# Optimization experiments

Measured on AMD Instinct MI355X. Metric: run time of the kernel, lower is better.

Reference implementation:

```python
import jax, jax.numpy as jnp
import numpy as np

N_NODES = 50000
N_EDGES = 800000
NODE_DIM = 27
HIDDEN = 64
CTX = 32
HEADS = 4
NEG_SLOPE = 0.2


def _gat_layer(x, src, dst, W, a_src, a_dst, bias, n_nodes):
    # x: [N, F_in], W: [F_in, H*C], a_src/a_dst: [H, C], bias: [C]
    h = (x @ W).reshape(n_nodes, HEADS, -1)            # [N, H, C]
    alpha_src = jnp.einsum('nhc,hc->nh', h, a_src)     # [N, H]
    alpha_dst = jnp.einsum('nhc,hc->nh', h, a_dst)     # [N, H]
    e = alpha_src[src] + alpha_dst[dst]                # [E, H]
    e = jax.nn.leaky_relu(e, NEG_SLOPE)
    # segment softmax over edges grouped by destination node
    e_max = jax.ops.segment_max(e, dst, num_segments=n_nodes)  # [N, H]
    e_exp = jnp.exp(e - e_max[dst])                    # [E, H]
    denom = jax.ops.segment_sum(e_exp, dst, num_segments=n_nodes)  # [N, H]
    alpha = e_exp / denom[dst]                         # [E, H]
    msg = alpha[:, :, None] * h[src]                   # [E, H, C]
    out = jax.ops.segment_sum(msg, dst, num_segments=n_nodes)      # [N, H, C]
    return out.mean(axis=1) + bias                     # concat=False -> head mean


def setup_inputs() -> dict:
    key = jax.random.key(0)
    ks = jax.random.split(key, 16)
    glorot = lambda k, shp: jax.random.normal(k, shp, jnp.float32) * jnp.sqrt(2.0 / (shp[0] + shp[-1]))
    inp = {
        'x': jax.random.normal(ks[0], (N_NODES, NODE_DIM), jnp.float32),
        'edge_index': jax.random.randint(ks[1], (2, N_EDGES), 0, N_NODES, jnp.int32),
        'donor_emb': jax.random.normal(ks[2], (1, CTX), jnp.float32),
        # GAT layer 1
        'W1': glorot(ks[3], (NODE_DIM, HEADS * HIDDEN)),
        'a_src1': glorot(ks[4], (HEADS, HIDDEN)),
        'a_dst1': glorot(ks[5], (HEADS, HIDDEN)),
        'b1': jnp.zeros((HIDDEN,), jnp.float32),
        # GAT layer 2
        'W2': glorot(ks[6], (HIDDEN, HEADS * HIDDEN)),
        'a_src2': glorot(ks[7], (HEADS, HIDDEN)),
        'a_dst2': glorot(ks[8], (HEADS, HIDDEN)),
        'b2': jnp.zeros((HIDDEN,), jnp.float32),
        # scorer MLP
        'Ws1': glorot(ks[9], (HIDDEN + CTX, HIDDEN)),
        'bs1': jnp.zeros((HIDDEN,), jnp.float32),
        'Ws2': glorot(ks[10], (HIDDEN, 1)),
        'bs2': jnp.zeros((1,), jnp.float32),
    }
    return inp


def reference(x, edge_index, donor_emb, W1, a_src1, a_dst1, b1,
              W2, a_src2, a_dst2, b2, Ws1, bs1, Ws2, bs2):
    n = x.shape[0]
    # PyG GATConv default add_self_loops=True
    loop = jnp.arange(n, dtype=edge_index.dtype)
    src = jnp.concatenate([edge_index[0], loop])
    dst = jnp.concatenate([edge_index[1], loop])

    h = jax.nn.elu(_gat_layer(x, src, dst, W1, a_src1, a_dst1, b1, n))
    h = jax.nn.elu(_gat_layer(h, src, dst, W2, a_src2, a_dst2, b2, n))

    ctx = jnp.concatenate([h, jnp.broadcast_to(donor_emb, (n, donor_emb.shape[-1]))], axis=-1)
    hidden = jax.nn.relu(ctx @ Ws1 + bs1)
    logits = (hidden @ Ws2 + bs2).squeeze(-1)          # [N]
    return logits
```

## Files before the change

### kernel.cpp

```cpp
#include <hip/hip_runtime.h>
#include <hip/hip_fp16.h>
#include <cmath>

#define HEADS 4
#define CH 64
#define HC 256
#define NEG 0.2f

typedef __attribute__((ext_vector_type(8))) short short8;
typedef __attribute__((ext_vector_type(4))) float f32x4;
typedef __fp16 half2_t __attribute__((ext_vector_type(2)));

__device__ __forceinline__ float leaky(float v){ return v > 0.f ? v : NEG * v; }

__device__ __forceinline__ short bf16_rne(float f){
    unsigned u = __float_as_uint(f);
    unsigned r = u + 0x7fffu + ((u >> 16) & 1u);
    return (short)(r >> 16);
}
__device__ __forceinline__ float bf16_to_f(short s){
    return __uint_as_float(((unsigned)(unsigned short)s) << 16);
}
__device__ __forceinline__ half2_t bc16(unsigned u){ return __builtin_bit_cast(half2_t, u); }
__device__ __forceinline__ unsigned packh2(float a, float b){
    __half ha = __float2half(a), hb = __float2half(b);
    return (unsigned)__builtin_bit_cast(unsigned short, ha)
         | ((unsigned)__builtin_bit_cast(unsigned short, hb) << 16);
}

__device__ __forceinline__ int block_excl_scan(int v, int* ws4){
    int tid = threadIdx.x, lane = tid & 63, wv = tid >> 6;
    int incl = v;
    #pragma unroll
    for (int off = 1; off < 64; off <<= 1){
        int t = __shfl_up(incl, off);
        if (lane >= off) incl += t;
    }
    if (lane == 63) ws4[wv] = incl;
    __syncthreads();
    int add = 0;
    for (int w = 0; w < wv; ++w) add += ws4[w];
    return incl - v + add;
}


__global__ __launch_bounds__(256) void prep_hist_kernel(
    const float* __restrict__ W1, const float* __restrict__ W2,
    const float* __restrict__ Ws1, const float* __restrict__ bs1,
    const float* __restrict__ donor,
    short* __restrict__ w1hi, short* __restrict__ w2hi,
    short* __restrict__ s1hi, short* __restrict__ s1lo,
    float* __restrict__ d1p,
    const int* __restrict__ ei, int E, int N, int NB, int* __restrict__ bucket_cnt)
{
    if ((int)blockIdx.x < 256){
        int t = blockIdx.x * 256 + threadIdx.x;
        int T = 256 * 256;
        for (int i = t; i < 256 * 40; i += T){
            int n = i / 40, k = i % 40;
            w1hi[i] = bf16_rne((k < 27) ? W1[(size_t)k * HC + n] : 0.f);
        }
        for (int i = t; i < 256 * 72; i += T){
            int n = i / 72, k = i % 72;
            w2hi[i] = bf16_rne((k < 64) ? W2[(size_t)k * HC + n] : 0.f);
        }
        for (int i = t; i < 64 * 72; i += T){
            int n = i / 72, k = i % 72;
            float v = (k < 64) ? Ws1[(size_t)k * 64 + n] : 0.f;
            short hi = bf16_rne(v);
            s1hi[i] = hi; s1lo[i] = bf16_rne(v - bf16_to_f(hi));
        }
        if (t < 64){
            float s = bs1[t];
            for (int k = 0; k < 32; ++k) s = fmaf(donor[k], Ws1[(size_t)(64 + k) * 64 + t], s);
            d1p[t] = s;
        }
    } else {
        __shared__ int lh[256];
        int tid = threadIdx.x;
        int ET = E + N;
        int ebase = ((int)blockIdx.x - 256) * 2048;
        lh[tid] = 0;
        __syncthreads();
        #pragma unroll
        for (int j = 0; j < 8; ++j){
            int e = ebase + j * 256 + tid;
            if (e < ET){
                int d = (e < E) ? ei[E + e] : (e - E);
                atomicAdd(&lh[d >> 8], 1);
            }
        }
        __syncthreads();
        if (tid < NB && lh[tid]) atomicAdd(&bucket_cnt[tid], lh[tid]);
    }
}


__global__ __launch_bounds__(256) void coarse_scatter_kernel(
    const int* __restrict__ ei, int E, int N, int NB,
    const int* __restrict__ bucket_cnt, int* __restrict__ bucket_cursor,
    unsigned* __restrict__ pairs)
{
    __shared__ int ws4[4];
    __shared__ int gbase[256];
    __shared__ int lh[256];
    __shared__ int gb[256];
    int tid = threadIdx.x;
    int ET = E + N;
    {
        int v = (tid < NB) ? bucket_cnt[tid] : 0;
        gbase[tid] = block_excl_scan(v, ws4);
    }
    lh[tid] = 0;
    __syncthreads();
    int ebase = blockIdx.x * 2048;
    int d[8], s[8], r[8];
    #pragma unroll
    for (int j = 0; j < 8; ++j){
        int e = ebase + j * 256 + tid;
        d[j] = -1;
        if (e < ET){
            if (e < E){ s[j] = ei[e]; d[j] = ei[E + e]; } else { s[j] = d[j] = e - E; }
            r[j] = atomicAdd(&lh[d[j] >> 8], 1);
        }
    }
    __syncthreads();
    if (tid < NB && lh[tid]) gb[tid] = gbase[tid] + atomicAdd(&bucket_cursor[tid], lh[tid]);
    __syncthreads();
    #pragma unroll
    for (int j = 0; j < 8; ++j){
        if (d[j] >= 0)
            pairs[gb[d[j] >> 8] + r[j]] = ((unsigned)d[j] << 16) | (unsigned)s[j];
    }
}


__device__ __forceinline__ void fine_sort_body(
    int b, const unsigned* __restrict__ pairs, const int* __restrict__ bucket_cnt, int NB,
    int* __restrict__ colsrc, int* __restrict__ rowptr, int N, int ET)
{
    __shared__ int ws4f[4];
    __shared__ int sb[257];
    __shared__ int hist[256];
    __shared__ int cur[256];
    int tid = threadIdx.x;
    {
        int v = (tid < NB) ? bucket_cnt[tid] : 0;
        int excl = block_excl_scan(v, ws4f);
        sb[tid] = excl;
        if (tid == 255) sb[256] = excl + v;
    }
    hist[tid] = 0;
    __syncthreads();
// ... 114 lines not shown
        }
    }

    #pragma unroll
    for (int r = 0; r < 4; ++r) {
        int n = n0 + wv * 16 + quad * 4 + r;
        if (n < N) {
            if (NT == 16) {
                #pragma unroll
                for (int q = 0; q < 4; ++q) {
                    uint2 u;
                    u.x = packh2(acc[q][r],     acc[q + 4][r]);
                    u.y = packh2(acc[q + 8][r], acc[q + 12][r]);
                    *(uint2*)((char*)h + (size_t)n * 512 + (q * 16 + ln) * 8) = u;
                }
            } else {
                #pragma unroll
                for (int q = 0; q < 4; ++q) {
                    unsigned u = packh2(acc[q][r], acc[q + 4][r]);
                    *(unsigned*)((char*)h + (size_t)n * 512 + (q * 16 + ln) * 8 + ((c0 >> 6) << 1)) = u;
                }
            }
        }
    }

    float aS[NT], aD[NT];
    #pragma unroll
    for (int nt = 0; nt < NT; ++nt) {
        aS[nt] = a_src[c0 + nt * 16 + ln];
        aD[nt] = a_dst[c0 + nt * 16 + ln];
    }
    #pragma unroll
    for (int hl = 0; hl < NT / 4; ++hl) {
        #pragma unroll
        for (int r = 0; r < 4; ++r) {
            float ps = 0.f, pd = 0.f;
            #pragma unroll
            for (int i = 0; i < 4; ++i) {
                ps = fmaf(acc[hl * 4 + i][r], aS[hl * 4 + i], ps);
                pd = fmaf(acc[hl * 4 + i][r], aD[hl * 4 + i], pd);
            }
            #pragma unroll
            for (int off = 1; off < 16; off <<= 1) {
                ps += __shfl_xor(ps, off);
                pd += __shfl_xor(pd, off);
            }
            if (ln == 0) {
                int n = n0 + wv * 16 + quad * 4 + r;
                if (n < N) {
                    int hg = c0 / 64 + hl;
                    asrc[n * 4 + hg] = ps;
                    adst[n * 4 + hg] = pd;
                }
            }
        }
    }
}

__global__ __launch_bounds__(256) void transform1_fine_kernel(
    const float* __restrict__ xin, const short* __restrict__ whi,
    const float* __restrict__ a_src, const float* __restrict__ a_dst,
    __half* __restrict__ h, float* __restrict__ asrc, float* __restrict__ adst, int N,
    int nblk, const unsigned* __restrict__ pairs, const int* __restrict__ bucket_cnt, int NB,
    int* __restrict__ colsrc, int* __restrict__ rowptr, int ET)
{
    if ((int)blockIdx.x < nblk) {
        transform_body<27, 1, 16, false, false>(blockIdx.x, 0, xin, whi, nullptr,
                                                a_src, a_dst, h, asrc, adst, N);
    } else {
        fine_sort_body(blockIdx.x - nblk, pairs, bucket_cnt, NB, colsrc, rowptr, N, ET);
    }
}

__global__ __launch_bounds__(256) void transform2_kernel(
    const float* __restrict__ xin, const short* __restrict__ whi,
    const float* __restrict__ a_src, const float* __restrict__ a_dst,
    __half* __restrict__ h, float* __restrict__ asrc, float* __restrict__ adst, int N)
{
    transform_body<64, 2, 16, false, true>(blockIdx.x, 0, xin, whi, nullptr,
                                           a_src, a_dst, h, asrc, adst, N);
}


__global__ __launch_bounds__(256) void aggregate_kernel(
    const int* __restrict__ rowptr, const int* __restrict__ colsrc,
    const __half* __restrict__ h, const float* __restrict__ asrc,
    const float* __restrict__ adst, const float* __restrict__ bias,
    float* __restrict__ hout, int N)
{
    int tid = threadIdx.x;
    int grp = tid >> 5;
    int lane32 = tid & 31;
    int n = blockIdx.x * 8 + grp;
    if (n >= N) return;
    int start = rowptr[n], end = rowptr[n + 1];
    int deg = end - start;
    const float4 ad = *(const float4*)(adst + (size_t)n * 4);

    int src0 = 0;
    float e0 = -1e30f, e1 = -1e30f, e2 = -1e30f, e3 = -1e30f;
    bool v0 = lane32 < deg;
    if (v0){
        src0 = colsrc[start + lane32];
        float4 as = *(const float4*)(asrc + (size_t)src0 * 4);
        e0 = leaky(as.x + ad.x); e1 = leaky(as.y + ad.y);
        e2 = leaky(as.z + ad.z); e3 = leaky(as.w + ad.w);
    }

    float m0, m1, m2, m3, i0, i1, i2, i3, p0, p1, p2, p3;
    if (deg <= 32){
        m0 = e0; m1 = e1; m2 = e2; m3 = e3;
        #pragma unroll
        for (int off = 1; off < 32; off <<= 1){
            m0 = fmaxf(m0, __shfl_xor(m0, off));
            m1 = fmaxf(m1, __shfl_xor(m1, off));
            m2 = fmaxf(m2, __shfl_xor(m2, off));
            m3 = fmaxf(m3, __shfl_xor(m3, off));
        }
        p0 = __expf(e0 - m0);
        p1 = __expf(e1 - m1);
        p2 = __expf(e2 - m2);
        p3 = __expf(e3 - m3);
        float t0 = p0, t1 = p1, t2 = p2, t3 = p3;
        #pragma unroll
        for (int off = 1; off < 32; off <<= 1){
            t0 += __shfl_xor(t0, off);
            t1 += __shfl_xor(t1, off);
            t2 += __shfl_xor(t2, off);
            t3 += __shfl_xor(t3, off);
        }
        i0 = 1.f / t0; i1 = 1.f / t1; i2 = 1.f / t2; i3 = 1.f / t3;
    } else {
        m0 = e0; m1 = e1; m2 = e2; m3 = e3;
        float t0 = v0 ? 1.f : 0.f, t1 = t0, t2 = t0, t3 = t0;
        for (int i = start + 32 + lane32; i < end; i += 32){
            int s = colsrc[i];
            float4 as = *(const float4*)(asrc + (size_t)s * 4);
            float e, nm;
            e = leaky(as.x + ad.x); nm = fmaxf(m0, e); t0 = t0 * __expf(m0 - nm) + __expf(e - nm); m0 = nm;
            e = leaky(as.y + ad.y); nm = fmaxf(m1, e); t1 = t1 * __expf(m1 - nm) + __expf(e - nm); m1 = nm;
            e = leaky(as.z + ad.z); nm = fmaxf(m2, e); t2 = t2 * __expf(m2 - nm) + __expf(e - nm); m2 = nm;
            e = leaky(as.w + ad.w); nm = fmaxf(m3, e); t3 = t3 * __expf(m3 - nm) + __expf(e - nm); m3 = nm;
        }
        #pragma unroll
        for (int off = 1; off < 32; off <<= 1){
            float om, os, nm;
            om = __shfl_xor(m0, off); os = __shfl_xor(t0, off);
            nm = fmaxf(m0, om); t0 = t0 * __expf(m0 - nm) + os * __expf(om - nm); m0 = nm;
            om = __shfl_xor(m1, off); os = __shfl_xor(t1, off);
            nm = fmaxf(m1, om); t1 = t1 * __expf(m1 - nm) + os * __expf(om - nm); m1 = nm;
            om = __shfl_xor(m2, off); os = __shfl_xor(t2, off);
            nm = fmaxf(m2, om); t2 = t2 * __expf(m2 - nm) + os * __expf(om - nm); m2 = nm;
            om = __shfl_xor(m3, off); os = __shfl_xor(t3, off);
            nm = fmaxf(m3, om); t3 = t3 * __expf(m3 - nm) + os * __expf(om - nm); m3 = nm;
        }
        i0 = 1.f / t0; i1 = 1.f / t1; i2 = 1.f / t2; i3 = 1.f / t3;
        p0 = __expf(e0 - m0); p1 = __expf(e1 - m1);
        p2 = __expf(e2 - m2); p3 = __expf(e3 - m3);
    }

    float accA = 0.f, accB = 0.f;
    const int boff = lane32 * 16;
    bool first = true;
    for (int base = start; base < end; base += 32){
        int cnt = end - base; if (cnt > 32) cnt = 32;
        float w0, w1, w2, w3; int off = 0;
        if (first){
            w0 = p0 * i0; w1 = p1 * i1; w2 = p2 * i2; w3 = p3 * i3;
            off = v0 ? src0 * (HC * 2) : 0;
        } else {
            w0 = w1 = w2 = w3 = 0.f;
            if (lane32 < cnt){
                int s = colsrc[base + lane32];
                float4 as = *(const float4*)(asrc + (size_t)s * 4);
                w0 = __expf(leaky(as.x + ad.x) - m0) * i0;
                w1 = __expf(leaky(as.y + ad.y) - m1) * i1;
                w2 = __expf(leaky(as.z + ad.z) - m2) * i2;
                w3 = __expf(leaky(as.w + ad.w) - m3) * i3;
                off = s * (HC * 2);
            }
        }
        first = false;
        half2_t q01 = __builtin_amdgcn_cvt_pkrtz(w0, w1);
        half2_t q23 = __builtin_amdgcn_cvt_pkrtz(w2, w3);
        unsigned wx = __builtin_bit_cast(unsigned, q01);
        unsigned wy = __builtin_bit_cast(unsigned, q23);

        int j = 0;
        for (; j + 2 <= cnt; j += 2){
            int o0 = __shfl(off, j, 32);
            unsigned a0 = __shfl((int)wx, j, 32), b0 = __shfl((int)wy, j, 32);
            int o1 = __shfl(off, j + 1, 32);
            unsigned a1 = __shfl((int)wx, j + 1, 32), b1 = __shfl((int)wy, j + 1, 32);
            uint4 h0 = *(const uint4*)((const char*)h + o0 + boff);
            uint4 h1 = *(const uint4*)((const char*)h + o1 + boff);
            accA = __builtin_amdgcn_fdot2(bc16(h0.x), bc16(a0), accA, false);
            accA = __builtin_amdgcn_fdot2(bc16(h0.y), bc16(b0), accA, false);
            accB = __builtin_amdgcn_fdot2(bc16(h0.z), bc16(a0), accB, false);
            accB = __builtin_amdgcn_fdot2(bc16(h0.w), bc16(b0), accB, false);
            accA = __builtin_amdgcn_fdot2(bc16(h1.x), bc16(a1), accA, false);
            accA = __builtin_amdgcn_fdot2(bc16(h1.y), bc16(b1), accA, false);
            accB = __builtin_amdgcn_fdot2(bc16(h1.z), bc16(a1), accB, false);
            accB = __builtin_amdgcn_fdot2(bc16(h1.w), bc16(b1), accB, false);
        }
        for (; j < cnt; ++j){
            int o0 = __shfl(off, j, 32);
            unsigned a0 = __shfl((int)wx, j, 32), b0 = __shfl((int)wy, j, 32);
            uint4 h0 = *(const uint4*)((const char*)h + o0 + boff);
            accA = __builtin_amdgcn_fdot2(bc16(h0.x), bc16(a0), accA, false);
            accA = __builtin_amdgcn_fdot2(bc16(h0.y), bc16(b0), accA, false);
            accB = __builtin_amdgcn_fdot2(bc16(h0.z), bc16(a0), accB, false);
            accB = __builtin_amdgcn_fdot2(bc16(h0.w), bc16(b0), accB, false);
        }
    }

    float2 bv = *(const float2*)(bias + lane32 * 2);
    float oA = accA * 0.25f + bv.x;
    float oB = accB * 0.25f + bv.y;
    oA = (oA > 0.f) ? oA : expm1f(oA);
    oB = (oB > 0.f) ? oB : expm1f(oB);
    *(float2*)(hout + (size_t)n * CH + lane32 * 2) = make_float2(oA, oB);
}


__global__ __launch_bounds__(256) void scorer_mfma_kernel(
    const float* __restrict__ h2, const short* __restrict__ s1hi, const short* __restrict__ s1lo,
    const float* __restrict__ d1p, const float* __restrict__ Ws2, const float* __restrict__ bs2,
    float* __restrict__ out, int N)
{
    constexpr int WP = 72;
    __shared__ short whi[64 * WP];
    __shared__ short wlo[64 * WP];
    const int tid = threadIdx.x;
    const int n0 = blockIdx.x * 64;

    const int wv = tid >> 6, lane = tid & 63;
    const int quad = lane >> 4, ln = lane & 15;
    const int myrow = wv * 16 + ln;
    const int nme = n0 + myrow;

    float fdir[16];
    #pragma unroll
    for (int ks = 0; ks < 2; ++ks){
        float4 f0 = make_float4(0.f, 0.f, 0.f, 0.f), f1 = f0;
        if (nme < N){
            const float* ap = h2 + (size_t)nme * 64 + ks * 32 + quad * 8;
            f0 = *(const float4*)ap;
            f1 = *(const float4*)(ap + 4);
        }
        fdir[ks*8+0]=f0.x; fdir[ks*8+1]=f0.y; fdir[ks*8+2]=f0.z; fdir[ks*8+3]=f0.w;
        fdir[ks*8+4]=f1.x; fdir[ks*8+5]=f1.y; fdir[ks*8+6]=f1.z; fdir[ks*8+7]=f1.w;
    }
    {
        const short8* ghi = (const short8*)s1hi;
        const short8* glo = (const short8*)s1lo;
        short8* lhi = (short8*)whi;
        short8* llo = (short8*)wlo;
        for (int t = tid; t < 64 * WP / 8; t += 256){ lhi[t] = ghi[t]; llo[t] = glo[t]; }
    }
    __syncthreads();

    f32x4 acc[4];
    #pragma unroll
    for (int i = 0; i < 4; ++i) acc[i] = (f32x4){0.f, 0.f, 0.f, 0.f};

    #pragma unroll
    for (int ks = 0; ks < 2; ++ks) {
        const int k0 = ks * 32 + quad * 8;
        short8 ahi, alo;
        #pragma unroll
        for (int e = 0; e < 8; ++e) {
            float v = fdir[ks * 8 + e];
            short hi = bf16_rne(v);
            ahi[e] = hi;
            alo[e] = bf16_rne(v - bf16_to_f(hi));
        }
        #pragma unroll
        for (int nt = 0; nt < 4; ++nt) {
            short8 bhi = *(const short8*)(whi + (nt * 16 + ln) * WP + k0);
            short8 blo = *(const short8*)(wlo + (nt * 16 + ln) * WP + k0);
            acc[nt] = __builtin_amdgcn_mfma_f32_16x16x32_bf16(ahi, bhi, acc[nt], 0, 0, 0);
            acc[nt] = __builtin_amdgcn_mfma_f32_16x16x32_bf16(alo, bhi, acc[nt], 0, 0, 0);
            acc[nt] = __builtin_amdgcn_mfma_f32_16x16x32_bf16(ahi, blo, acc[nt], 0, 0, 0);
        }
    }

    float d1v[4], w2v[4];
    #pragma unroll
    for (int nt = 0; nt < 4; ++nt){
        d1v[nt] = d1p[nt * 16 + ln];
        w2v[nt] = Ws2[nt * 16 + ln];
    }
    float b2 = bs2[0];
    #pragma unroll
    for (int r = 0; r < 4; ++r){
        float t = 0.f;
        #pragma unroll
        for (int nt = 0; nt < 4; ++nt)
            t = fmaf(fmaxf(acc[nt][r] + d1v[nt], 0.f), w2v[nt], t);
        #pragma unroll
        for (int off = 1; off < 16; off <<= 1) t += __shfl_xor(t, off);
        if (ln == 0){
            int n = n0 + wv * 16 + quad * 4 + r;
            if (n < N) out[n] = t + b2;
        }
    }
}


extern "C" void kernel_launch(void* const* d_in, const int* in_sizes, int n_in,
                              void* d_out, int out_size, void* d_ws, size_t ws_size,
                              hipStream_t stream)
{
    const float* x    = (const float*)d_in[0];
    const int*   ei   = (const int*)  d_in[1];
    const float* donor= (const float*)d_in[2];
    const float* W1   = (const float*)d_in[3];
    const float* as1  = (const float*)d_in[4];
    const float* ad1  = (const float*)d_in[5];
    const float* b1   = (const float*)d_in[6];
    const float* W2   = (const float*)d_in[7];
    const float* as2  = (const float*)d_in[8];
    const float* ad2  = (const float*)d_in[9];
    const float* b2   = (const float*)d_in[10];
    const float* Ws1  = (const float*)d_in[11];
    const float* bs1  = (const float*)d_in[12];
    const float* Ws2  = (const float*)d_in[13];
    const float* bs2  = (const float*)d_in[14];

    const int N  = in_sizes[0] / 27;
    const int E  = in_sizes[1] / 2;
    const int ET = E + N;
    const int NB = (N + 255) / 256;

    char* ws = (char*)d_ws;
    auto alloc = [&](size_t bytes) -> void* {
        void* p = (void*)ws;
        ws += (bytes + 255) / 256 * 256;
        return p;
    };
    int*      rowptr  = (int*)     alloc((size_t)(N + 1) * 4);
    int*      colsrc  = (int*)     alloc((size_t)ET * 4);
    unsigned* pairs   = (unsigned*)alloc((size_t)ET * 4);
    __half*   hbig    = (__half*)  alloc((size_t)N * HC * 2);
    float*    asrc    = (float*)   alloc((size_t)N * 4 * 4);
    float*    adst    = (float*)   alloc((size_t)N * 4 * 4);
    float*    hmid    = (float*)   alloc((size_t)N * CH * 4);
    int*      bucket_cnt    = (int*) alloc(256 * 4);
    int*      bucket_cursor = (int*) alloc(256 * 4);
    short*    w1hi    = (short*)   alloc(256 * 40 * 2);
    short*    w2hi    = (short*)   alloc(256 * 72 * 2);
    short*    s1hi    = (short*)   alloc(64 * 72 * 2);
    short*    s1lo    = (short*)   alloc(64 * 72 * 2);
    float*    d1p     = (float*)   alloc(64 * 4);

    const int nblk = (N + 63) / 64;
    const int hblk = (ET + 2047) / 2048;

    (void)hipMemsetAsync(bucket_cnt, 0, 512 * 4, stream);
    prep_hist_kernel<<<256 + hblk, 256, 0, stream>>>(W1, W2, Ws1, bs1, donor,
        w1hi, w2hi, s1hi, s1lo, d1p, ei, E, N, NB, bucket_cnt);
    coarse_scatter_kernel<<<hblk, 256, 0, stream>>>(ei, E, N, NB, bucket_cnt, bucket_cursor, pairs);
    transform1_fine_kernel<<<nblk + NB, 256, 0, stream>>>(
        x, w1hi, as1, ad1, hbig, asrc, adst, N,
        nblk, pairs, bucket_cnt, NB, colsrc, rowptr, ET);
    aggregate_kernel<<<(N + 7) / 8, 256, 0, stream>>>(
        rowptr, colsrc, hbig, asrc, adst, b1, hmid, N);
    transform2_kernel<<<nblk, 256, 0, stream>>>(
        hmid, w2hi, as2, ad2, hbig, asrc, adst, N);
    aggregate_kernel<<<(N + 7) / 8, 256, 0, stream>>>(
        rowptr, colsrc, hbig, asrc, adst, b2, hmid, N);
    scorer_mfma_kernel<<<nblk, 256, 0, stream>>>(
        hmid, s1hi, s1lo, d1p, Ws2, bs2, (float*)d_out, N);
}
```

Baseline: 285.6 us.

## Prefetch neighbor rows into LDS with async ring buffer in aggregate

For nodes with degree at most 32, the aggregate kernel now uses global_load_lds to stream gathered neighbor feature rows into a per-wave 8-slot LDS ring. Manual vmcnt and lgkmcnt waits keep up to eight gathers in flight while earlier rows are read back and accumulated with fdot2. It also splits accumulation into two independent chains and computes normalized weights directly. The intent is to hide the latency of the irregular gathers, at the cost of hand-written wait counts, extra LDS use per block and wasted prefetches past the end of short neighbor lists.

```diff
diff --git a/kernel.cpp b/kernel.cpp
--- a/kernel.cpp
+++ b/kernel.cpp
@@ -10,6 +10,9 @@
 typedef __attribute__((ext_vector_type(8))) short short8;
 typedef __attribute__((ext_vector_type(4))) float f32x4;
 typedef __fp16 half2_t __attribute__((ext_vector_type(2)));
+typedef __attribute__((address_space(3))) char lds_char_t;
+typedef __attribute__((address_space(3))) void lds_void_t;
+typedef const __attribute__((address_space(1))) void g_void_t;
 
 __device__ __forceinline__ float leaky(float v){ return v > 0.f ? v : NEG * v; }
 
@@ -26,6 +29,18 @@
     __half ha = __float2half(a), hb = __float2half(b);
     return (unsigned)__builtin_bit_cast(unsigned short, ha)
          | ((unsigned)__builtin_bit_cast(unsigned short, hb) << 16);
+}
+__device__ __forceinline__ float fd2(unsigned hv, unsigned w, float acc){
+    return __builtin_amdgcn_fdot2(bc16(hv), bc16(w), acc, false);
+}
+
+__device__ __forceinline__ void gload_lds16(const void* g, void* l){
+    __builtin_amdgcn_global_load_lds((g_void_t*)g, (lds_void_t*)l, 16, 0, 0);
+}
+__device__ __forceinline__ uint4 lds_read_b128(unsigned addr){
+    uint4 r;
+    asm volatile("ds_read_b128 %0, %1" : "=v"(r) : "v"(addr));
+    return r;
 }
 
 __device__ __forceinline__ int block_excl_scan(int v, int* ws4){
@@ -355,7 +370,10 @@
     const float* __restrict__ adst, const float* __restrict__ bias,
     float* __restrict__ hout, int N)
 {
+    __shared__ char stage[4][8 * 1024];
     int tid = threadIdx.x;
+    int wv = tid >> 6;
+    int lane = tid & 63;
     int grp = tid >> 5;
     int lane32 = tid & 31;
     int n = blockIdx.x * 8 + grp;
@@ -374,9 +392,11 @@
         e2 = leaky(as.z + ad.z); e3 = leaky(as.w + ad.w);
     }
 
-    float m0, m1, m2, m3, i0, i1, i2, i3, p0, p1, p2, p3;
+    float accA = 0.f, accB = 0.f;
+    const int boff = lane32 * 16;
+
     if (deg <= 32){
-        m0 = e0; m1 = e1; m2 = e2; m3 = e3;
+        float m0 = e0, m1 = e1, m2 = e2, m3 = e3;
         #pragma unroll
         for (int off = 1; off < 32; off <<= 1){
             m0 = fmaxf(m0, __shfl_xor(m0, off));
@@ -384,10 +404,10 @@
             m2 = fmaxf(m2, __shfl_xor(m2, off));
             m3 = fmaxf(m3, __shfl_xor(m3, off));
         }
-        p0 = __expf(e0 - m0);
-        p1 = __expf(e1 - m1);
-        p2 = __expf(e2 - m2);
-        p3 = __expf(e3 - m3);
+        float p0 = __expf(e0 - m0);
+        float p1 = __expf(e1 - m1);
+        float p2 = __expf(e2 - m2);
+        float p3 = __expf(e3 - m3);
         float t0 = p0, t1 = p1, t2 = p2, t3 = p3;
         #pragma unroll
         for (int off = 1; off < 32; off <<= 1){
@@ -396,9 +416,58 @@
             t2 += __shfl_xor(t2, off);
             t3 += __shfl_xor(t3, off);
         }
-        i0 = 1.f / t0; i1 = 1.f / t1; i2 = 1.f / t2; i3 = 1.f / t3;
+        half2_t q01 = __builtin_amdgcn_cvt_pkrtz(p0 / t0, p1 / t1);
+        half2_t q23 = __builtin_amdgcn_cvt_pkrtz(p2 / t2, p3 / t3);
+        int wx = (int)__builtin_bit_cast(unsigned, q01);
+        int wy = (int)__builtin_bit_cast(unsigned, q23);
+        int offv = v0 ? src0 * (HC * 2) : 0;
+
+        const char* hb = (const char*)h;
+        char* sbg = &stage[wv][0];
+        unsigned sb_off = (unsigned)(size_t)(lds_char_t*)sbg;
+        unsigned my_off = sb_off + (unsigned)lane * 16u;
+
+        #pragma unroll
+        for (int p = 0; p < 8; ++p){
+            int o = __shfl(offv, p, 32);
+            gload_lds16(hb + o + boff, sbg + p * 1024);
+        }
+
+        float accA1 = 0.f, accB1 = 0.f;
+        int j = 0;
+        for (; j + 2 <= deg; j += 2){
+            asm volatile("s_waitcnt vmcnt(7)" ::: "memory");
+            uint4 h0 = lds_read_b128(my_off + (unsigned)((j & 7) * 1024));
+            asm volatile("s_waitcnt lgkmcnt(0)" ::: "memory");
+            __builtin_amdgcn_sched_barrier(0);
+            { int o = __shfl(offv, (j + 8) & 31, 32);
+              gload_lds16(hb + o + boff, sbg + (j & 7) * 1024); }
+            asm volatile("s_waitcnt vmcnt(7)" ::: "memory");
+            uint4 h1 = lds_read_b128(my_off + (unsigned)(((j + 1) & 7) * 1024));
+            asm volatile("s_waitcnt lgkmcnt(0)" ::: "memory");
+            __builtin_amdgcn_sched_barrier(0);
+            { int o = __shfl(offv, (j + 9) & 31, 32);
+              gload_lds16(hb + o + boff, sbg + ((j + 1) & 7) * 1024); }
+            unsigned a0 = (unsigned)__shfl(wx, j, 32),     c0 = (unsigned)__shfl(wy, j, 32);
+            unsigned a1 = (unsigned)__shfl(wx, j + 1, 32), c1 = (unsigned)__shfl(wy, j + 1, 32);
+            accA  = fd2(h0.x, a0, accA);  accA  = fd2(h0.y, c0, accA);
+            accB  = fd2(h0.z, a0, accB);  accB  = fd2(h0.w, c0, accB);
+            accA1 = fd2(h1.x, a1, accA1); accA1 = fd2(h1.y, c1, accA1);
+            accB1 = fd2(h1.z, a1, accB1); accB1 = fd2(h1.w, c1, accB1);
+        }
+        if (j < deg){
+            asm volatile("s_waitcnt vmcnt(7)" ::: "memory");
+            uint4 h0 = lds_read_b128(my_off + (unsigned)((j & 7) * 1024));
+            asm volatile("s_waitcnt lgkmcnt(0)" ::: "memory");
+            __builtin_amdgcn_sched_barrier(0);
+            unsigned a0 = (unsigned)__shfl(wx, j, 32), c0 = (unsigned)__shfl(wy, j, 32);
+            accA = fd2(h0.x, a0, accA); accA = fd2(h0.y, c0, accA);
+            accB = fd2(h0.z, a0, accB); accB = fd2(h0.w, c0, accB);
+        }
+        asm volatile("s_waitcnt vmcnt(0)" ::: "memory");
+        accA += accA1; accB += accB1;
     } else {
-        m0 = e0; m1 = e1; m2 = e2; m3 = e3;
+        float m0 = e0, m1 = e1, m2 = e2, m3 = e3;
         float t0 = v0 ? 1.f : 0.f, t1 = t0, t2 = t0, t3 = t0;
         for (int i = start + 32 + lane32; i < end; i += 32){
             int s = colsrc[i];
@@ -421,63 +490,55 @@
             om = __shfl_xor(m3, off); os = __shfl_xor(t3, off);
             nm = fmaxf(m3, om); t3 = t3 * __expf(m3 - nm) + os * __expf(om - nm); m3 = nm;
         }
-        i0 = 1.f / t0; i1 = 1.f / t1; i2 = 1.f / t2; i3 = 1.f / t3;
-        p0 = __expf(e0 - m0); p1 = __expf(e1 - m1);
-        p2 = __expf(e2 - m2); p3 = __expf(e3 - m3);
-    }
-
-    float accA = 0.f, accB = 0.f;
-    const int boff = lane32 * 16;
-    bool first = true;
-    for (int base = start; base < end; base += 32){
-        int cnt = end - base; if (cnt > 32) cnt = 32;
-        float w0, w1, w2, w3; int off = 0;
-        if (first){
-            w0 = p0 * i0; w1 = p1 * i1; w2 = p2 * i2; w3 = p3 * i3;
-            off = v0 ? src0 * (HC * 2) : 0;
-        } else {
-            w0 = w1 = w2 = w3 = 0.f;
-            if (lane32 < cnt){
-                int s = colsrc[base + lane32];
-                float4 as = *(const float4*)(asrc + (size_t)s * 4);
-                w0 = __expf(leaky(as.x + ad.x) - m0) * i0;
-                w1 = __expf(leaky(as.y + ad.y) - m1) * i1;
-                w2 = __expf(leaky(as.z + ad.z) - m2) * i2;
-                w3 = __expf(leaky(as.w + ad.w) - m3) * i3;
-                off = s * (HC * 2);
-            }
-        }
-        first = false;
-        half2_t q01 = __builtin_amdgcn_cvt_pkrtz(w0, w1);
-        half2_t q23 = __builtin_amdgcn_cvt_pkrtz(w2, w3);
-        unsigned wx = __builtin_bit_cast(unsigned, q01);
-        unsigned wy = __builtin_bit_cast(unsigned, q23);
-
-        int j = 0;
-        for (; j + 2 <= cnt; j += 2){
-            int o0 = __shfl(off, j, 32);
-            unsigned a0 = __shfl((int)wx, j, 32), b0 = __shfl((int)wy, j, 32);
-            int o1 = __shfl(off, j + 1, 32);
-            unsigned a1 = __shfl((int)wx, j + 1, 32), b1 = __shfl((int)wy, j + 1, 32);
-            uint4 h0 = *(const uint4*)((const char*)h + o0 + boff);
-            uint4 h1 = *(const uint4*)((const char*)h + o1 + boff);
-            accA = __builtin_amdgcn_fdot2(bc16(h0.x), bc16(a0), accA, false);
-            accA = __builtin_amdgcn_fdot2(bc16(h0.y), bc16(b0), accA, false);
-            accB = __builtin_amdgcn_fdot2(bc16(h0.z), bc16(a0), accB, false);
-            accB = __builtin_amdgcn_fdot2(bc16(h0.w), bc16(b0), accB, false);
-            accA = __builtin_amdgcn_fdot2(bc16(h1.x), bc16(a1), accA, false);
-            accA = __builtin_amdgcn_fdot2(bc16(h1.y), bc16(b1), accA, false);
-            accB = __builtin_amdgcn_fdot2(bc16(h1.z), bc16(a1), accB, false);
-            accB = __builtin_amdgcn_fdot2(bc16(h1.w), bc16(b1), accB, false);
-        }
-        for (; j < cnt; ++j){
-            int o0 = __shfl(off, j, 32);
-            unsigned a0 = __shfl((int)wx, j, 32), b0 = __shfl((int)wy, j, 32);
-            uint4 h0 = *(const uint4*)((const char*)h + o0 + boff);
-            accA = __builtin_amdgcn_fdot2(bc16(h0.x), bc16(a0), accA, false);
-            accA = __builtin_amdgcn_fdot2(bc16(h0.y), bc16(b0), accA, false);
-            accB = __builtin_amdgcn_fdot2(bc16(h0.z), bc16(a0), accB, false);
-            accB = __builtin_amdgcn_fdot2(bc16(h0.w), bc16(b0), accB, false);
+        float i0 = 1.f / t0, i1 = 1.f / t1, i2 = 1.f / t2, i3 = 1.f / t3;
+        float p0 = __expf(e0 - m0), p1 = __expf(e1 - m1);
+        float p2 = __expf(e2 - m2), p3 = __expf(e3 - m3);
+
+        bool first = true;
+        for (int base = start; base < end; base += 32){
+            int cnt = end - base; if (cnt > 32) cnt = 32;
+            float w0, w1, w2, w3; int off = 0;
+            if (first){
+                w0 = p0 * i0; w1 = p1 * i1; w2 = p2 * i2; w3 = p3 * i3;
+                off = v0 ? src0 * (HC * 2) : 0;
+            } else {
+                w0 = w1 = w2 = w3 = 0.f;
+                if (lane32 < cnt){
+                    int s = colsrc[base + lane32];
+                    float4 as = *(const float4*)(asrc + (size_t)s * 4);
+                    w0 = __expf(leaky(as.x + ad.x) - m0) * i0;
+                    w1 = __expf(leaky(as.y + ad.y) - m1) * i1;
+                    w2 = __expf(leaky(as.z + ad.z) - m2) * i2;
+                    w3 = __expf(leaky(as.w + ad.w) - m3) * i3;
+                    off = s * (HC * 2);
+                }
+            }
+            first = false;
+            half2_t q01 = __builtin_amdgcn_cvt_pkrtz(w0, w1);
+            half2_t q23 = __builtin_amdgcn_cvt_pkrtz(w2, w3);
+            unsigned wx = __builtin_bit_cast(unsigned, q01);
+            unsigned wy = __builtin_bit_cast(unsigned, q23);
+
+            int j = 0;
+            for (; j + 2 <= cnt; j += 2){
+                int o0 = __shfl(off, j, 32);
+                unsigned a0 = __shfl((int)wx, j, 32), b0 = __shfl((int)wy, j, 32);
+                int o1 = __shfl(off, j + 1, 32);
+                unsigned a1 = __shfl((int)wx, j + 1, 32), b1 = __shfl((int)wy, j + 1, 32);
+                uint4 h0 = *(const uint4*)((const char*)h + o0 + boff);
+                uint4 h1 = *(const uint4*)((const char*)h + o1 + boff);
+                accA = fd2(h0.x, a0, accA); accA = fd2(h0.y, b0, accA);
+                accB = fd2(h0.z, a0, accB); accB = fd2(h0.w, b0, accB);
+                accA = fd2(h1.x, a1, accA); accA = fd2(h1.y, b1, accA);
+                accB = fd2(h1.z, a1, accB); accB = fd2(h1.w, b1, accB);
+            }
+            for (; j < cnt; ++j){
+                int o0 = __shfl(off, j, 32);
+                unsigned a0 = __shfl((int)wx, j, 32), b0 = __shfl((int)wy, j, 32);
+                uint4 h0 = *(const uint4*)((const char*)h + o0 + boff);
+                accA = fd2(h0.x, a0, accA); accA = fd2(h0.y, b0, accA);
+                accB = fd2(h0.z, a0, accB); accB = fd2(h0.w, b0, accB);
+            }
         }
     }
 
```

Result: slower. 298.6 us (+4.6%).

## Split GAT aggregation into edge-alpha pass and channel-sliced gather kernel

Applied to the files above, without the earlier changes.

The fused softmax+gather aggregate kernel becomes two kernels. The first computes per-edge attention weights and stores them as packed fp16 in a new workspace buffer. The second gathers h using 8 channel-slice blocks per node chunk, with 4 threads per node. Slicing by channel is meant to shrink each block's gather working set so the fp16 h table (N×256 halves) gets better L2 reuse. In exchange it adds an extra launch, an 8-byte-per-edge alpha write and read, and re-reads colsrc and alpha once per slice.

```diff
diff --git a/kernel.cpp b/kernel.cpp
--- a/kernel.cpp
+++ b/kernel.cpp
@@ -26,6 +26,9 @@
     __half ha = __float2half(a), hb = __float2half(b);
     return (unsigned)__builtin_bit_cast(unsigned short, ha)
          | ((unsigned)__builtin_bit_cast(unsigned short, hb) << 16);
+}
+__device__ __forceinline__ float fd2(unsigned hv, unsigned w, float acc){
+    return __builtin_amdgcn_fdot2(bc16(hv), bc16(w), acc, false);
 }
 
 __device__ __forceinline__ int block_excl_scan(int v, int* ws4){
@@ -349,11 +352,10 @@
 }
 
 
-__global__ __launch_bounds__(256) void aggregate_kernel(
+__global__ __launch_bounds__(256) void edge_alpha_kernel(
     const int* __restrict__ rowptr, const int* __restrict__ colsrc,
-    const __half* __restrict__ h, const float* __restrict__ asrc,
-    const float* __restrict__ adst, const float* __restrict__ bias,
-    float* __restrict__ hout, int N)
+    const float* __restrict__ asrc, const float* __restrict__ adst,
+    uint2* __restrict__ alpha, int N)
 {
     int tid = threadIdx.x;
     int grp = tid >> 5;
@@ -364,19 +366,17 @@
     int deg = end - start;
     const float4 ad = *(const float4*)(adst + (size_t)n * 4);
 
-    int src0 = 0;
     float e0 = -1e30f, e1 = -1e30f, e2 = -1e30f, e3 = -1e30f;
     bool v0 = lane32 < deg;
     if (v0){
-        src0 = colsrc[start + lane32];
-        float4 as = *(const float4*)(asrc + (size_t)src0 * 4);
+        int s = colsrc[start + lane32];
+        float4 as = *(const float4*)(asrc + (size_t)s * 4);
         e0 = leaky(as.x + ad.x); e1 = leaky(as.y + ad.y);
         e2 = leaky(as.z + ad.z); e3 = leaky(as.w + ad.w);
     }
 
-    float m0, m1, m2, m3, i0, i1, i2, i3, p0, p1, p2, p3;
     if (deg <= 32){
-        m0 = e0; m1 = e1; m2 = e2; m3 = e3;
+        float m0 = e0, m1 = e1, m2 = e2, m3 = e3;
         #pragma unroll
         for (int off = 1; off < 32; off <<= 1){
             m0 = fmaxf(m0, __shfl_xor(m0, off));
@@ -384,10 +384,10 @@
             m2 = fmaxf(m2, __shfl_xor(m2, off));
             m3 = fmaxf(m3, __shfl_xor(m3, off));
         }
-        p0 = __expf(e0 - m0);
-        p1 = __expf(e1 - m1);
-        p2 = __expf(e2 - m2);
-        p3 = __expf(e3 - m3);
+        float p0 = __expf(e0 - m0);
+        float p1 = __expf(e1 - m1);
+        float p2 = __expf(e2 - m2);
+        float p3 = __expf(e3 - m3);
         float t0 = p0, t1 = p1, t2 = p2, t3 = p3;
         #pragma unroll
         for (int off = 1; off < 32; off <<= 1){
@@ -396,9 +396,16 @@
             t2 += __shfl_xor(t2, off);
             t3 += __shfl_xor(t3, off);
         }
-        i0 = 1.f / t0; i1 = 1.f / t1; i2 = 1.f / t2; i3 = 1.f / t3;
+        if (v0){
+            half2_t q01 = __builtin_amdgcn_cvt_pkrtz(p0 / t0, p1 / t1);
+            half2_t q23 = __builtin_amdgcn_cvt_pkrtz(p2 / t2, p3 / t3);
+            uint2 w;
+            w.x = __builtin_bit_cast(unsigned, q01);
+            w.y = __builtin_bit_cast(unsigned, q23);
+            alpha[start + lane32] = w;
+        }
     } else {
-        m0 = e0; m1 = e1; m2 = e2; m3 = e3;
+        float m0 = e0, m1 = e1, m2 = e2, m3 = e3;
         float t0 = v0 ? 1.f : 0.f, t1 = t0, t2 = t0, t3 = t0;
         for (int i = start + 32 + lane32; i < end; i += 32){
             int s = colsrc[i];
@@ -421,72 +428,84 @@
             om = __shfl_xor(m3, off); os = __shfl_xor(t3, off);
             nm = fmaxf(m3, om); t3 = t3 * __expf(m3 - nm) + os * __expf(om - nm); m3 = nm;
         }
-        i0 = 1.f / t0; i1 = 1.f / t1; i2 = 1.f / t2; i3 = 1.f / t3;
-        p0 = __expf(e0 - m0); p1 = __expf(e1 - m1);
-        p2 = __expf(e2 - m2); p3 = __expf(e3 - m3);
-    }
-
-    float accA = 0.f, accB = 0.f;
-    const int boff = lane32 * 16;
-    bool first = true;
-    for (int base = start; base < end; base += 32){
-        int cnt = end - base; if (cnt > 32) cnt = 32;
-        float w0, w1, w2, w3; int off = 0;
-        if (first){
-            w0 = p0 * i0; w1 = p1 * i1; w2 = p2 * i2; w3 = p3 * i3;
-            off = v0 ? src0 * (HC * 2) : 0;
-        } else {
-            w0 = w1 = w2 = w3 = 0.f;
-            if (lane32 < cnt){
+        float i0 = 1.f / t0, i1 = 1.f / t1, i2 = 1.f / t2, i3 = 1.f / t3;
+
+        bool first = true;
+        for (int base = start; base < end; base += 32){
+            int cnt = end - base; if (cnt > 32) cnt = 32;
+            float w0 = 0.f, w1 = 0.f, w2 = 0.f, w3 = 0.f;
+            if (first){
+                w0 = __expf(e0 - m0) * i0; w1 = __expf(e1 - m1) * i1;
+                w2 = __expf(e2 - m2) * i2; w3 = __expf(e3 - m3) * i3;
+            } else if (lane32 < cnt){
                 int s = colsrc[base + lane32];
                 float4 as = *(const float4*)(asrc + (size_t)s * 4);
                 w0 = __expf(leaky(as.x + ad.x) - m0) * i0;
                 w1 = __expf(leaky(as.y + ad.y) - m1) * i1;
                 w2 = __expf(leaky(as.z + ad.z) - m2) * i2;
                 w3 = __expf(leaky(as.w + ad.w) - m3) * i3;
-                off = s * (HC * 2);
-            }
-        }
-        first = false;
-        half2_t q01 = __builtin_amdgcn_cvt_pkrtz(w0, w1);
-        half2_t q23 = __builtin_amdgcn_cvt_pkrtz(w2, w3);
-        unsigned wx = __builtin_bit_cast(unsigned, q01);
-        unsigned wy = __builtin_bit_cast(unsigned, q23);
-
-        int j = 0;
-        for (; j + 2 <= cnt; j += 2){
-            int o0 = __shfl(off, j, 32);
-            unsigned a0 = __shfl((int)wx, j, 32), b0 = __shfl((int)wy, j, 32);
-            int o1 = __shfl(off, j + 1, 32);
-            unsigned a1 = __shfl((int)wx, j + 1, 32), b1 = __shfl((int)wy, j + 1, 32);
-            uint4 h0 = *(const uint4*)((const char*)h + o0 + boff);
-            uint4 h1 = *(const uint4*)((const char*)h + o1 + boff);
-            accA = __builtin_amdgcn_fdot2(bc16(h0.x), bc16(a0), accA, false);
-            accA = __builtin_amdgcn_fdot2(bc16(h0.y), bc16(b0), accA, false);
-            accB = __builtin_amdgcn_fdot2(bc16(h0.z), bc16(a0), accB, false);
-            accB = __builtin_amdgcn_fdot2(bc16(h0.w), bc16(b0), accB, false);
-            accA = __builtin_amdgcn_fdot2(bc16(h1.x), bc16(a1), accA, false);
-            accA = __builtin_amdgcn_fdot2(bc16(h1.y), bc16(b1), accA, false);
-            accB = __builtin_amdgcn_fdot2(bc16(h1.z), bc16(a1), accB, false);
-            accB = __builtin_amdgcn_fdot2(bc16(h1.w), bc16(b1), accB, false);
-        }
-        for (; j < cnt; ++j){
-            int o0 = __shfl(off, j, 32);
-            unsigned a0 = __shfl((int)wx, j, 32), b0 = __shfl((int)wy, j, 32);
-            uint4 h0 = *(const uint4*)((const char*)h + o0 + boff);
-            accA = __builtin_amdgcn_fdot2(bc16(h0.x), bc16(a0), accA, false);
-            accA = __builtin_amdgcn_fdot2(bc16(h0.y), bc16(b0), accA, false);
-            accB = __builtin_amdgcn_fdot2(bc16(h0.z), bc16(a0), accB, false);
-            accB = __builtin_amdgcn_fdot2(bc16(h0.w), bc16(b0), accB, false);
-        }
-    }
-
-    float2 bv = *(const float2*)(bias + lane32 * 2);
+            }
+            first = false;
+            if (lane32 < cnt){
+                half2_t q01 = __builtin_amdgcn_cvt_pkrtz(w0, w1);
+                half2_t q23 = __builtin_amdgcn_cvt_pkrtz(w2, w3);
+                uint2 w;
+                w.x = __builtin_bit_cast(unsigned, q01);
+                w.y = __builtin_bit_cast(unsigned, q23);
+                alpha[base + lane32] = w;
+            }
+        }
+    }
+}
+
+
+__global__ __launch_bounds__(256) void aggregate_slice_kernel(
+    const int* __restrict__ rowptr, const int* __restrict__ colsrc,
+    const uint2* __restrict__ alpha, const __half* __restrict__ h,
+    const float* __restrict__ bias, float* __restrict__ hout, int N)
+{
+    int tid = threadIdx.x;
+    int slice = blockIdx.x & 7;
+    int chunk = blockIdx.x >> 3;
+    int q = tid & 3;
+    int n = chunk * 64 + (tid >> 2);
+    if (n >= N) return;
+    int start = rowptr[n], end = rowptr[n + 1];
+    const char* hb = (const char*)h;
+    const int sboff = slice * 64 + q * 16;
+
+    float accA = 0.f, accB = 0.f;
+    for (int base = start; base < end; base += 32){
+        int cnt = end - base; if (cnt > 32) cnt = 32;
+        int cs[8]; unsigned alx[8], aly[8];
+        #pragma unroll
+        for (int k = 0; k < 8; ++k){
+            int idx = base + q + 4 * k;
+            if (idx > end - 1) idx = end - 1;
+            cs[k] = colsrc[idx] * 512;
+            uint2 a = alpha[idx];
+            alx[k] = a.x; aly[k] = a.y;
+        }
+        #pragma unroll
+        for (int e = 0; e < 32; ++e){
+            if (e < cnt){
+                int o = __shfl(cs[e >> 2], e & 3, 4);
+                unsigned wA = (unsigned)__shfl((int)alx[e >> 2], e & 3, 4);
+                unsigned wB = (unsigned)__shfl((int)aly[e >> 2], e & 3, 4);
+                uint4 hv = *(const uint4*)(hb + o + sboff);
+                accA = fd2(hv.x, wA, accA); accA = fd2(hv.y, wB, accA);
+                accB = fd2(hv.z, wA, accB); accB = fd2(hv.w, wB, accB);
+            }
+        }
+    }
+
+    int c = slice * 8 + q * 2;
+    float2 bv = *(const float2*)(bias + c);
     float oA = accA * 0.25f + bv.x;
     float oB = accB * 0.25f + bv.y;
     oA = (oA > 0.f) ? oA : expm1f(oA);
     oB = (oB > 0.f) ? oB : expm1f(oB);
-    *(float2*)(hout + (size_t)n * CH + lane32 * 2) = make_float2(oA, oB);
+    *(float2*)(hout + (size_t)n * CH + c) = make_float2(oA, oB);
 }
 
 
@@ -613,6 +632,7 @@
     float*    asrc    = (float*)   alloc((size_t)N * 4 * 4);
     float*    adst    = (float*)   alloc((size_t)N * 4 * 4);
     float*    hmid    = (float*)   alloc((size_t)N * CH * 4);
+    uint2*    alpha   = (uint2*)   alloc((size_t)ET * 8);
     int*      bucket_cnt    = (int*) alloc(256 * 4);
     int*      bucket_cursor = (int*) alloc(256 * 4);
     short*    w1hi    = (short*)   alloc(256 * 40 * 2);
@@ -623,6 +643,7 @@
 
     const int nblk = (N + 63) / 64;
     const int hblk = (ET + 2047) / 2048;
+    const int sblk = 8 * ((N + 63) / 64);
 
     (void)hipMemsetAsync(bucket_cnt, 0, 512 * 4, stream);
     prep_hist_kernel<<<256 + hblk, 256, 0, stream>>>(W1, W2, Ws1, bs1, donor,
@@ -631,12 +652,16 @@
     transform1_fine_kernel<<<nblk + NB, 256, 0, stream>>>(
         x, w1hi, as1, ad1, hbig, asrc, adst, N,
         nblk, pairs, bucket_cnt, NB, colsrc, rowptr, ET);
-    aggregate_kernel<<<(N + 7) / 8, 256, 0, stream>>>(
-        rowptr, colsrc, hbig, asrc, adst, b1, hmid, N);
+    edge_alpha_kernel<<<(N + 7) / 8, 256, 0, stream>>>(
+        rowptr, colsrc, asrc, adst, alpha, N);
+    aggregate_slice_kernel<<<sblk, 256, 0, stream>>>(
+        rowptr, colsrc, alpha, hbig, b1, hmid, N);
     transform2_kernel<<<nblk, 256, 0, stream>>>(
         hmid, w2hi, as2, ad2, hbig, asrc, adst, N);
-    aggregate_kernel<<<(N + 7) / 8, 256, 0, stream>>>(
-        rowptr, colsrc, hbig, asrc, adst, b2, hmid, N);
+    edge_alpha_kernel<<<(N + 7) / 8, 256, 0, stream>>>(
+        rowptr, colsrc, asrc, adst, alpha, N);
+    aggregate_slice_kernel<<<sblk, 256, 0, stream>>>(
+        rowptr, colsrc, alpha, hbig, b2, hmid, N);
     scorer_mfma_kernel<<<nblk, 256, 0, stream>>>(
         hmid, s1hi, s1lo, d1p, Ws2, bs2, (float*)d_out, N);
 }
```

Result: slower. 361.5 us (+26.6%).

## Fuse scorer MLP into second aggregation kernel epilogue

Applied to the files above, without the earlier changes.

Removes the separate MFMA scorer kernel and its bf16 hi/lo weight preparation, and computes the scorer MLP in the epilogue of the second aggregate kernel. Each block loads the 64x64 Ws1 slice (16 KB) into shared memory, and each 32-lane group computes the hidden layer with shuffles and FMAs, then reduces against Ws2. This saves one launch and the write and re-read of the N x 64 layer-2 output. In exchange it adds a 16 KB shared load per 8-node block (6250 blocks) plus scalar FMA work, and the larger shared footprint may reduce occupancy of the gather-bound kernel.

```diff
diff --git a/kernel.cpp b/kernel.cpp
--- a/kernel.cpp
+++ b/kernel.cpp
@@ -27,6 +27,9 @@
     return (unsigned)__builtin_bit_cast(unsigned short, ha)
          | ((unsigned)__builtin_bit_cast(unsigned short, hb) << 16);
 }
+__device__ __forceinline__ float fd2(unsigned hv, unsigned w, float acc){
+    return __builtin_amdgcn_fdot2(bc16(hv), bc16(w), acc, false);
+}
 
 __device__ __forceinline__ int block_excl_scan(int v, int* ws4){
     int tid = threadIdx.x, lane = tid & 63, wv = tid >> 6;
@@ -49,7 +52,6 @@
     const float* __restrict__ Ws1, const float* __restrict__ bs1,
     const float* __restrict__ donor,
     short* __restrict__ w1hi, short* __restrict__ w2hi,
-    short* __restrict__ s1hi, short* __restrict__ s1lo,
     float* __restrict__ d1p,
     const int* __restrict__ ei, int E, int N, int NB, int* __restrict__ bucket_cnt)
 {
@@ -63,12 +65,6 @@
         for (int i = t; i < 256 * 72; i += T){
             int n = i / 72, k = i % 72;
             w2hi[i] = bf16_rne((k < 64) ? W2[(size_t)k * HC + n] : 0.f);
-        }
-        for (int i = t; i < 64 * 72; i += T){
-            int n = i / 72, k = i % 72;
-            float v = (k < 64) ? Ws1[(size_t)k * 64 + n] : 0.f;
-            short hi = bf16_rne(v);
-            s1hi[i] = hi; s1lo[i] = bf16_rne(v - bf16_to_f(hi));
         }
         if (t < 64){
             float s = bs1[t];
@@ -349,17 +345,30 @@
 }
 
 
+template<int SCORE>
 __global__ __launch_bounds__(256) void aggregate_kernel(
     const int* __restrict__ rowptr, const int* __restrict__ colsrc,
     const __half* __restrict__ h, const float* __restrict__ asrc,
     const float* __restrict__ adst, const float* __restrict__ bias,
-    float* __restrict__ hout, int N)
-{
+    float* __restrict__ hout, int N,
+    const float* __restrict__ Ws1g, const float* __restrict__ d1pg,
+    const float* __restrict__ Ws2g, const float* __restrict__ bs2g,
+    float* __restrict__ outg)
+{
+    __shared__ float ws1L[SCORE ? 4096 : 8];
     int tid = threadIdx.x;
     int grp = tid >> 5;
     int lane32 = tid & 31;
     int n = blockIdx.x * 8 + grp;
+
+    if (SCORE){
+        const float4* g = (const float4*)Ws1g;
+        float4* l = (float4*)ws1L;
+        for (int t = tid; t < 1024; t += 256) l[t] = g[t];
+        __syncthreads();
+    }
     if (n >= N) return;
+
     int start = rowptr[n], end = rowptr[n + 1];
     int deg = end - start;
     const float4 ad = *(const float4*)(adst + (size_t)n * 4);
@@ -461,23 +470,17 @@
             unsigned a1 = __shfl((int)wx, j + 1, 32), b1 = __shfl((int)wy, j + 1, 32);
             uint4 h0 = *(const uint4*)((const char*)h + o0 + boff);
             uint4 h1 = *(const uint4*)((const char*)h + o1 + boff);
-            accA = __builtin_amdgcn_fdot2(bc16(h0.x), bc16(a0), accA, false);
-            accA = __builtin_amdgcn_fdot2(bc16(h0.y), bc16(b0), accA, false);
-            accB = __builtin_amdgcn_fdot2(bc16(h0.z), bc16(a0), accB, false);
-            accB = __builtin_amdgcn_fdot2(bc16(h0.w), bc16(b0), accB, false);
-            accA = __builtin_amdgcn_fdot2(bc16(h1.x), bc16(a1), accA, false);
-            accA = __builtin_amdgcn_fdot2(bc16(h1.y), bc16(b1), accA, false);
-            accB = __builtin_amdgcn_fdot2(bc16(h1.z), bc16(a1), accB, false);
-            accB = __builtin_amdgcn_fdot2(bc16(h1.w), bc16(b1), accB, false);
+            accA = fd2(h0.x, a0, accA); accA = fd2(h0.y, b0, accA);
+            accB = fd2(h0.z, a0, accB); accB = fd2(h0.w, b0, accB);
+            accA = fd2(h1.x, a1, accA); accA = fd2(h1.y, b1, accA);
+            accB = fd2(h1.z, a1, accB); accB = fd2(h1.w, b1, accB);
         }
         for (; j < cnt; ++j){
             int o0 = __shfl(off, j, 32);
             unsigned a0 = __shfl((int)wx, j, 32), b0 = __shfl((int)wy, j, 32);
             uint4 h0 = *(const uint4*)((const char*)h + o0 + boff);
-            accA = __builtin_amdgcn_fdot2(bc16(h0.x), bc16(a0), accA, false);
-            accA = __builtin_amdgcn_fdot2(bc16(h0.y), bc16(b0), accA, false);
-            accB = __builtin_amdgcn_fdot2(bc16(h0.z), bc16(a0), accB, false);
-            accB = __builtin_amdgcn_fdot2(bc16(h0.w), bc16(b0), accB, false);
+            accA = fd2(h0.x, a0, accA); accA = fd2(h0.y, b0, accA);
+            accB = fd2(h0.z, a0, accB); accB = fd2(h0.w, b0, accB);
         }
     }
 
@@ -486,91 +489,25 @@
     float oB = accB * 0.25f + bv.y;
     oA = (oA > 0.f) ? oA : expm1f(oA);
     oB = (oB > 0.f) ? oB : expm1f(oB);
-    *(float2*)(hout + (size_t)n * CH + lane32 * 2) = make_float2(oA, oB);
-}
-
-
-__global__ __launch_bounds__(256) void scorer_mfma_kernel(
-    const float* __restrict__ h2, const short* __restrict__ s1hi, const short* __restrict__ s1lo,
-    const float* __restrict__ d1p, const float* __restrict__ Ws2, const float* __restrict__ bs2,
-    float* __restrict__ out, int N)
-{
-    constexpr int WP = 72;
-    __shared__ short whi[64 * WP];
-    __shared__ short wlo[64 * WP];
-    const int tid = threadIdx.x;
-    const int n0 = blockIdx.x * 64;
-
-    const int wv = tid >> 6, lane = tid & 63;
-    const int quad = lane >> 4, ln = lane & 15;
-    const int myrow = wv * 16 + ln;
-    const int nme = n0 + myrow;
-
-    float fdir[16];
-    #pragma unroll
-    for (int ks = 0; ks < 2; ++ks){
-        float4 f0 = make_float4(0.f, 0.f, 0.f, 0.f), f1 = f0;
-        if (nme < N){
-            const float* ap = h2 + (size_t)nme * 64 + ks * 32 + quad * 8;
-            f0 = *(const float4*)ap;
-            f1 = *(const float4*)(ap + 4);
-        }
-        fdir[ks*8+0]=f0.x; fdir[ks*8+1]=f0.y; fdir[ks*8+2]=f0.z; fdir[ks*8+3]=f0.w;
-        fdir[ks*8+4]=f1.x; fdir[ks*8+5]=f1.y; fdir[ks*8+6]=f1.z; fdir[ks*8+7]=f1.w;
-    }
-    {
-        const short8* ghi = (const short8*)s1hi;
-        const short8* glo = (const short8*)s1lo;
-        short8* lhi = (short8*)whi;
-        short8* llo = (short8*)wlo;
-        for (int t = tid; t < 64 * WP / 8; t += 256){ lhi[t] = ghi[t]; llo[t] = glo[t]; }
-    }
-    __syncthreads();
-
-    f32x4 acc[4];
-    #pragma unroll
-    for (int i = 0; i < 4; ++i) acc[i] = (f32x4){0.f, 0.f, 0.f, 0.f};
-
-    #pragma unroll
-    for (int ks = 0; ks < 2; ++ks) {
-        const int k0 = ks * 32 + quad * 8;
-        short8 ahi, alo;
-        #pragma unroll
-        for (int e = 0; e < 8; ++e) {
-            float v = fdir[ks * 8 + e];
-            short hi = bf16_rne(v);
-            ahi[e] = hi;
-            alo[e] = bf16_rne(v - bf16_to_f(hi));
-        }
-        #pragma unroll
-        for (int nt = 0; nt < 4; ++nt) {
-            short8 bhi = *(const short8*)(whi + (nt * 16 + ln) * WP + k0);
-            short8 blo = *(const short8*)(wlo + (nt * 16 + ln) * WP + k0);
-            acc[nt] = __builtin_amdgcn_mfma_f32_16x16x32_bf16(ahi, bhi, acc[nt], 0, 0, 0);
-            acc[nt] = __builtin_amdgcn_mfma_f32_16x16x32_bf16(alo, bhi, acc[nt], 0, 0, 0);
-            acc[nt] = __builtin_amdgcn_mfma_f32_16x16x32_bf16(ahi, blo, acc[nt], 0, 0, 0);
-        }
-    }
-
-    float d1v[4], w2v[4];
-    #pragma unroll
-    for (int nt = 0; nt < 4; ++nt){
-        d1v[nt] = d1p[nt * 16 + ln];
-        w2v[nt] = Ws2[nt * 16 + ln];
-    }
-    float b2 = bs2[0];
-    #pragma unroll
-    for (int r = 0; r < 4; ++r){
-        float t = 0.f;
-        #pragma unroll
-        for (int nt = 0; nt < 4; ++nt)
-            t = fmaf(fmaxf(acc[nt][r] + d1v[nt], 0.f), w2v[nt], t);
-        #pragma unroll
-        for (int off = 1; off < 16; off <<= 1) t += __shfl_xor(t, off);
-        if (ln == 0){
-            int n = n0 + wv * 16 + quad * 4 + r;
-            if (n < N) out[n] = t + b2;
-        }
+
+    if (SCORE){
+        float ha = d1pg[lane32], hb = d1pg[lane32 + 32];
+        #pragma unroll
+        for (int l = 0; l < 32; ++l){
+            float va = __shfl(oA, l, 32);
+            float vb = __shfl(oB, l, 32);
+            ha = fmaf(va, ws1L[(2 * l) * 64 + lane32], ha);
+            ha = fmaf(vb, ws1L[(2 * l + 1) * 64 + lane32], ha);
+            hb = fmaf(va, ws1L[(2 * l) * 64 + lane32 + 32], hb);
+            hb = fmaf(vb, ws1L[(2 * l + 1) * 64 + lane32 + 32], hb);
+        }
+        ha = fmaxf(ha, 0.f); hb = fmaxf(hb, 0.f);
+        float t = fmaf(ha, Ws2g[lane32], hb * Ws2g[lane32 + 32]);
+        #pragma unroll
+        for (int off = 1; off < 32; off <<= 1) t += __shfl_xor(t, off);
+        if (lane32 == 0) outg[n] = t + bs2g[0];
+    } else {
+        *(float2*)(hout + (size_t)n * CH + lane32 * 2) = make_float2(oA, oB);
     }
 }
 
@@ -617,8 +554,6 @@
     int*      bucket_cursor = (int*) alloc(256 * 4);
     short*    w1hi    = (short*)   alloc(256 * 40 * 2);
     short*    w2hi    = (short*)   alloc(256 * 72 * 2);
-    short*    s1hi    = (short*)   alloc(64 * 72 * 2);
-    short*    s1lo    = (short*)   alloc(64 * 72 * 2);
     float*    d1p     = (float*)   alloc(64 * 4);
 
     const int nblk = (N + 63) / 64;
@@ -626,17 +561,17 @@
 
     (void)hipMemsetAsync(bucket_cnt, 0, 512 * 4, stream);
     prep_hist_kernel<<<256 + hblk, 256, 0, stream>>>(W1, W2, Ws1, bs1, donor,
-        w1hi, w2hi, s1hi, s1lo, d1p, ei, E, N, NB, bucket_cnt);
+        w1hi, w2hi, d1p, ei, E, N, NB, bucket_cnt);
     coarse_scatter_kernel<<<hblk, 256, 0, stream>>>(ei, E, N, NB, bucket_cnt, bucket_cursor, pairs);
     transform1_fine_kernel<<<nblk + NB, 256, 0, stream>>>(
         x, w1hi, as1, ad1, hbig, asrc, adst, N,
         nblk, pairs, bucket_cnt, NB, colsrc, rowptr, ET);
-    aggregate_kernel<<<(N + 7) / 8, 256, 0, stream>>>(
-        rowptr, colsrc, hbig, asrc, adst, b1, hmid, N);
+    aggregate_kernel<0><<<(N + 7) / 8, 256, 0, stream>>>(
+        rowptr, colsrc, hbig, asrc, adst, b1, hmid, N,
+        nullptr, nullptr, nullptr, nullptr, nullptr);
     transform2_kernel<<<nblk, 256, 0, stream>>>(
         hmid, w2hi, as2, ad2, hbig, asrc, adst, N);
-    aggregate_kernel<<<(N + 7) / 8, 256, 0, stream>>>(
-        rowptr, colsrc, hbig, asrc, adst, b2, hmid, N);
-    scorer_mfma_kernel<<<nblk, 256, 0, stream>>>(
-        hmid, s1hi, s1lo, d1p, Ws2, bs2, (float*)d_out, N);
-}
+    aggregate_kernel<1><<<(N + 7) / 8, 256, 0, stream>>>(
+        rowptr, colsrc, hbig, asrc, adst, b2, nullptr, N,
+        Ws1, d1p, Ws2, bs2, (float*)d_out);
+}
```

Result: slower. 298.8 us (+4.6%).
